# Optimization experiments

Hardware: AMD Instinct MI355X
Metric: run time of the kernel (lower is better)

The kernel has to match this reference:

```python
import jax, jax.numpy as jnp
import numpy as np

HEADS = 8
BUCKETS = 64
TEMP = 0.75
SINKHORN_ITER = 5
EPS = 1e-6


def setup_inputs() -> dict:
    key = jax.random.key(0)
    ks = jax.random.split(key, 6)
    b, t, d = 2, 4096, 1024
    x = jax.random.normal(ks[0], (b, t, d), dtype=jnp.float32)
    gumbel_u = jax.random.uniform(ks[1], (b * HEADS, BUCKETS, BUCKETS), dtype=jnp.float32)
    w_qkv = jax.random.normal(ks[2], (d, 3 * d), dtype=jnp.float32) * (d ** -0.5)
    sort_w = jax.random.normal(ks[3], (1, HEADS, (d // HEADS) * 2, BUCKETS), dtype=jnp.float32)
    w_out = jax.random.normal(ks[4], (d, d), dtype=jnp.float32) * (d ** -0.5)
    b_out = jax.random.normal(ks[5], (d,), dtype=jnp.float32) * 0.01
    return {"x": x, "gumbel_u": gumbel_u, "w_qkv": w_qkv, "sort_w": sort_w,
            "w_out": w_out, "b_out": b_out}


def reference(x, gumbel_u, w_qkv, sort_w, w_out, b_out):
    b, t, d = x.shape
    h, buckets = HEADS, BUCKETS
    d_h = d // h
    bsz = t // buckets
    bh = b * h

    # qkv projection (no bias) and head merge -> (b*h, t, d_h)
    qkv = x @ w_qkv
    q, k, v = jnp.split(qkv, 3, axis=2)
    def merge_heads(u):
        return u.reshape(b, t, h, d_h).transpose(0, 2, 1, 3).reshape(bh, t, d_h)
    q, k, v = merge_heads(q), merge_heads(k), merge_heads(v)

    # bucket -> (bh, buckets, bsz, d_h)
    b_q = q.reshape(bh, buckets, bsz, d_h)
    b_k = k.reshape(bh, buckets, bsz, d_h)
    b_v = v.reshape(bh, buckets, bsz, d_h)

    # SortNet: bucket sums -> leaky_relu(x @ W), W per-head (2*d_h, buckets)
    sx = jnp.concatenate([b_q.sum(axis=2), b_k.sum(axis=2)], axis=-1)  # (bh, buckets, 2*d_h)
    W = jnp.broadcast_to(sort_w, (b, h, 2 * d_h, buckets)).reshape(bh, 2 * d_h, buckets)
    R = jax.nn.leaky_relu(jnp.einsum('bue,bec->buc', sx, W), negative_slope=0.01)

    # gumbel-sinkhorn (log clamped for finiteness; matches torch when R >= 0)
    g = -jnp.log(-jnp.log(gumbel_u + EPS) + EPS)
    r = (jnp.log(jnp.maximum(R + EPS, EPS)) + g) / TEMP
    for _ in range(SINKHORN_ITER):
        r = r - jax.nn.logsumexp(r, axis=2, keepdims=True)
        r = r - jax.nn.logsumexp(r, axis=1, keepdims=True)
    R = jnp.exp(r)

    # zero all but top-1 along last dim
    idx = jnp.argmax(R, axis=2)
    R = jnp.where(jnp.arange(buckets)[None, None, :] == idx[..., None], R, 0.0)

    # soft-permute buckets of k and v, concat with locals -> (bh, buckets, 2*bsz, d_h)
    k_r = jnp.einsum('buv,bvtd->butd', R, b_k)
    v_r = jnp.einsum('buv,bvtd->butd', R, b_v)
    b_k2 = jnp.concatenate([k_r, b_k], axis=2)
    b_v2 = jnp.concatenate([v_r, b_v], axis=2)

    # bucketed attention; NOTE: scale uses full model dim d (as in source)
    dots = jnp.einsum('buie,buje->buij', b_q, b_k2) * (d ** -0.5)
    attn = jax.nn.softmax(dots, axis=-1)
    out = jnp.einsum('buij,buje->buie', attn, b_v2)  # (bh, buckets, bsz, d_h)

    out = out.reshape(b, h, t, d_h).transpose(0, 2, 1, 3).reshape(b, t, d)
    return out @ w_out + b_out
```

## Files before the change

kernel.cpp:

```cpp
#include <hip/hip_runtime.h>
#include <stdint.h>

#define TEMP_ 0.75f
#define EPS_ 1e-6f

typedef __attribute__((ext_vector_type(8))) short bf16x8;
typedef __attribute__((ext_vector_type(4))) float f32x4;

typedef __attribute__((address_space(1))) void gvoid_t;
typedef __attribute__((address_space(3))) void lvoid_t;

__device__ __forceinline__ void async_ld16(const void* g, void* l) {
  __builtin_amdgcn_global_load_lds((gvoid_t*)g, (lvoid_t*)l, 16, 0, 0);
}

__device__ __forceinline__ float b2f(ushort u) {
  return __builtin_bit_cast(float, (uint32_t)u << 16);
}
__device__ __forceinline__ ushort f2b(float f) {
  uint32_t x = __builtin_bit_cast(uint32_t, f);
  x += 0x7fffu + ((x >> 16) & 1u);
  return (ushort)(x >> 16);
}

__global__ __launch_bounds__(256) void prep_x(
    const float* __restrict__ x, ushort* __restrict__ xb, float* __restrict__ xsum2) {
  const int blk = blockIdx.x;
  const int bu = blk >> 1, half = blk & 1;
  const int b = bu >> 6, u = bu & 63;
  const int c = threadIdx.x * 4;
  const float* src = x + ((size_t)(b * 4096 + u * 64 + half * 32)) * 1024 + c;
  ushort* dst = xb + ((size_t)(b * 4096 + u * 64 + half * 32)) * 1024 + c;
  float s0 = 0.f, s1 = 0.f, s2 = 0.f, s3 = 0.f;
  for (int pos = 0; pos < 32; pos++) {
    float4 v = *(const float4*)(src + (size_t)pos * 1024);
    s0 += v.x; s1 += v.y; s2 += v.z; s3 += v.w;
    ushort4 o;
    o.x = f2b(v.x); o.y = f2b(v.y); o.z = f2b(v.z); o.w = f2b(v.w);
    *(ushort4*)(dst + (size_t)pos * 1024) = o;
  }
  float4 sv = {s0, s1, s2, s3};
  *(float4*)&xsum2[(size_t)blk * 1024 + c] = sv;
}

__global__ __launch_bounds__(256) void transpose_f2b(
    const float* __restrict__ src, ushort* __restrict__ dst, int R, int C) {
  __shared__ float tile[32][33];
  int bx = blockIdx.x * 32;
  int by = blockIdx.y * 32;
  int tx = threadIdx.x & 31, ty = threadIdx.x >> 5;
  #pragma unroll
  for (int i = 0; i < 32; i += 8)
    tile[ty + i][tx] = src[(size_t)(by + ty + i) * C + bx + tx];
  __syncthreads();
  #pragma unroll
  for (int i = 0; i < 32; i += 8)
    dst[(size_t)(bx + ty + i) * R + by + tx] = f2b(tile[tx][ty + i]);
}

__global__ __launch_bounds__(256) void sx_gemm_partial(
    const float* __restrict__ xsum2, const float* __restrict__ wqkv,
    float* __restrict__ SXP) {
  __shared__ float xs[128 * 8];
  const int cb = blockIdx.x;
  const int rt = blockIdx.y;
  const int kc = blockIdx.z;
  const int tid = threadIdx.x;
  for (int idx = tid; idx < 1024; idx += 256) {
    int k = idx >> 3, r = idx & 7;
    int bu = rt * 8 + r;
    int kk = kc * 128 + k;
    xs[idx] = xsum2[(size_t)(bu * 2) * 1024 + kk] + xsum2[(size_t)(bu * 2 + 1) * 1024 + kk];
  }
  __syncthreads();
  const int n = cb * 256 + tid;
  float acc[8];
  #pragma unroll
  for (int r = 0; r < 8; r++) acc[r] = 0.f;
  for (int k = 0; k < 128; k++) {
    float w = wqkv[(size_t)(kc * 128 + k) * 3072 + n];
    float4 a0 = *(const float4*)&xs[k * 8];
    float4 a1 = *(const float4*)&xs[k * 8 + 4];
    acc[0] += a0.x * w; acc[1] += a0.y * w; acc[2] += a0.z * w; acc[3] += a0.w * w;
    acc[4] += a1.x * w; acc[5] += a1.y * w; acc[6] += a1.z * w; acc[7] += a1.w * w;
  }
  #pragma unroll
  for (int r = 0; r < 8; r++)
    SXP[(size_t)(kc * 128 + rt * 8 + r) * 2048 + n] = acc[r];
}

__global__ __launch_bounds__(256) void sx_reduce(
    const float* __restrict__ SXP, float* __restrict__ SX) {
  const int bu = blockIdx.y;
  const int n = blockIdx.x * 256 + threadIdx.x;
  float s = 0.f;
  #pragma unroll
  for (int kc = 0; kc < 8; kc++)
    s += SXP[(size_t)(kc * 128 + bu) * 2048 + n];
  const int head = (n >> 7) & 7;
  const int e2 = ((n >> 10) << 7) | (n & 127);
  const int b = bu >> 6, u = bu & 63;
  SX[((size_t)((b * 8 + head) * 256) + e2) * 64 + u] = s;
}

__global__ __launch_bounds__(256) void sortnet_sinkhorn(
    const float* __restrict__ SX, const float* __restrict__ sortw,
    const float* __restrict__ gum, int* __restrict__ idxArr,
    float* __restrict__ wgtArr) {
  __shared__ float sxl[64 * 64];
  __shared__ float wl[64 * 64];
  __shared__ float rr[64 * 65];
  __shared__ float redA[256];
  __shared__ float redB[256];
  __shared__ int redi[256];
  const int bh = blockIdx.x, tid = threadIdx.x, head = bh & 7;
  const int ui = tid & 15, ci = tid >> 4;

  float acc[4][4];
  #pragma unroll
  for (int i = 0; i < 4; i++)
    #pragma unroll
    for (int j = 0; j < 4; j++) acc[i][j] = 0.f;

  const f32x4* SX4 = (const f32x4*)(SX + (size_t)bh * 16384);
  const f32x4* W4 = (const f32x4*)(sortw + (size_t)head * 16384);
  f32x4* sxl4 = (f32x4*)sxl;
  f32x4* wl4 = (f32x4*)wl;

  #pragma unroll 1
  for (int ch = 0; ch < 4; ch++) {
    __syncthreads();
    #pragma unroll 1
    for (int g = tid; g < 1024; g += 256) {
      sxl4[g] = SX4[ch * 1024 + g];
      wl4[g] = W4[ch * 1024 + g];
    }
    __syncthreads();
    #pragma unroll 2
    for (int e = 0; e < 64; e++) {
      f32x4 a = sxl4[e * 16 + ui];
      f32x4 w = wl4[e * 16 + ci];
      #pragma unroll
      for (int i = 0; i < 4; i++)
        #pragma unroll
        for (int j = 0; j < 4; j++) acc[i][j] += a[i] * w[j];
    }
  }

  #pragma unroll
  for (int i = 0; i < 4; i++)
    #pragma unroll
    for (int j = 0; j < 4; j++) {
      int u = ui * 4 + i, c = ci * 4 + j;
      float dot = acc[i][j];
      float r0 = dot > 0.f ? dot : 0.01f * dot;
      float gu = gum[(size_t)bh * 4096 + u * 64 + c];
      float inner = -logf(gu + EPS_) + EPS_;
      float g = -logf(fmaxf(inner, 1e-38f));
      rr[u * 65 + c] = (logf(fmaxf(r0 + EPS_, EPS_)) + g) / TEMP_;
    }
  __syncthreads();

  const int su = tid & 63, sq = tid >> 6;
  #pragma unroll 1
  for (int it = 0; it < 5; it++) {
    {
      float pm = -1e30f;
      #pragma unroll
      for (int j = 0; j < 16; j++) pm = fmaxf(pm, rr[su * 65 + sq * 16 + j]);
      redA[sq * 64 + su] = pm;
      __syncthreads();
      float m = fmaxf(fmaxf(redA[su], redA[64 + su]), fmaxf(redA[128 + su], redA[192 + su]));
      float ps = 0.f;
      #pragma unroll
      for (int j = 0; j < 16; j++) ps += expf(rr[su * 65 + sq * 16 + j] - m);
      redB[sq * 64 + su] = ps;
      __syncthreads();
      float l = m + logf(redB[su] + redB[64 + su] + redB[128 + su] + redB[192 + su]);
      #pragma unroll
      for (int j = 0; j < 16; j++) rr[su * 65 + sq * 16 + j] -= l;
      __syncthreads();
    }
    {
      float pm = -1e30f;
      #pragma unroll
      for (int j = 0; j < 16; j++) pm = fmaxf(pm, rr[(sq * 16 + j) * 65 + su]);
      redA[sq * 64 + su] = pm;
      __syncthreads();
      float m = fmaxf(fmaxf(redA[su], redA[64 + su]), fmaxf(redA[128 + su], redA[192 + su]));
      float ps = 0.f;
      #pragma unroll
      for (int j = 0; j < 16; j++) ps += expf(rr[(sq * 16 + j) * 65 + su] - m);
      redB[sq * 64 + su] = ps;
      __syncthreads();
      float l = m + logf(redB[su] + redB[64 + su] + redB[128 + su] + redB[192 + su]);
      #pragma unroll
      for (int j = 0; j < 16; j++) rr[(sq * 16 + j) * 65 + su] -= l;
      __syncthreads();
    }
  }

  {
    float pv = -1e30f;
    int pi = 0;
    #pragma unroll
    for (int j = 0; j < 16; j++) {
      float v = rr[su * 65 + sq * 16 + j];
      if (v > pv) { pv = v; pi = sq * 16 + j; }
    }
    redA[sq * 64 + su] = pv;
    redi[sq * 64 + su] = pi;
    __syncthreads();
    if (tid < 64) {
      float best = -1e30f;
      int bi = 0;
      #pragma unroll
      for (int q = 0; q < 4; q++) {
        float v = redA[q * 64 + tid];
        if (v > best) { best = v; bi = redi[q * 64 + tid]; }
      }
      idxArr[bh * 64 + tid] = bi;
      wgtArr[bh * 64 + tid] = expf(fminf(best, 80.f));
    }
  }
}

__global__ __launch_bounds__(256, 2) void gemm_bt(
    const ushort* __restrict__ A, const ushort* __restrict__ BT,
    int M, int N, int K, int mode,
    const float* __restrict__ bias, float* __restrict__ Cout,
    ushort* __restrict__ Qb, ushort* __restrict__ Kb, ushort* __restrict__ VT) {
  __shared__ ushort As_lo[128 * 32];
  __shared__ ushort As_hi[128 * 32];
  __shared__ ushort Bs_lo[128 * 32];
  __shared__ ushort Bs_hi[128 * 32];
  const int tid = threadIdx.x;
  const int wave = tid >> 6, lane = tid & 63;
  const int quad = lane >> 4, l16 = lane & 15;
  const int m0 = blockIdx.y * 128, n0 = blockIdx.x * 128;
  const int wm = (wave >> 1) * 64, wn = (wave & 1) * 64;

  f32x4 acc[4][4];
  #pragma unroll
  for (int i = 0; i < 4; i++)
    #pragma unroll
    for (int j = 0; j < 4; j++) acc[i][j] = (f32x4){0.f, 0.f, 0.f, 0.f};

  const int srow = wave * 32 + (lane >> 2);
  const int schunk = (lane & 3) * 8;

  for (int k0 = 0; k0 < K; k0 += 64) {
    __syncthreads();
    {
      const ushort* gA0 = A + (uint64_t)(m0 + srow) * K + k0 + schunk;
      const ushort* gB0 = BT + (uint64_t)(n0 + srow) * K + k0 + schunk;
      const int lofs = (wave * 32) * 32;
      async_ld16(gA0, (ushort*)As_lo + lofs);
      async_ld16(gA0 + (uint64_t)16 * K, (ushort*)As_lo + lofs + 16 * 32);
      async_ld16(gA0 + 32, (ushort*)As_hi + lofs);
      async_ld16(gA0 + (uint64_t)16 * K + 32, (ushort*)As_hi + lofs + 16 * 32);
      async_ld16(gB0, (ushort*)Bs_lo + lofs);
      async_ld16(gB0 + (uint64_t)16 * K, (ushort*)Bs_lo + lofs + 16 * 32);
      async_ld16(gB0 + 32, (ushort*)Bs_hi + lofs);
      async_ld16(gB0 + (uint64_t)16 * K + 32, (ushort*)Bs_hi + lofs + 16 * 32);
    }
    __syncthreads();
    #pragma unroll
    for (int kk = 0; kk < 2; kk++) {
      const ushort* Ab = kk ? As_hi : As_lo;
      const ushort* Bb = kk ? Bs_hi : Bs_lo;
      bf16x8 af[4], bfr[4];
      #pragma unroll
      for (int mt = 0; mt < 4; mt++)
        af[mt] = *(const bf16x8*)&Ab[(wm + mt * 16 + l16) * 32 + quad * 8];
      #pragma unroll
      for (int nt = 0; nt < 4; nt++)
        bfr[nt] = *(const bf16x8*)&Bb[(wn + nt * 16 + l16) * 32 + quad * 8];
      #pragma unroll
      for (int mt = 0; mt < 4; mt++)
        #pragma unroll
        for (int nt = 0; nt < 4; nt++)
          acc[mt][nt] = __builtin_amdgcn_mfma_f32_16x16x32_bf16(af[mt], bfr[nt], acc[mt][nt], 0, 0, 0);
    }
  }

  if (mode == 0) {
    #pragma unroll
    for (int mt = 0; mt < 4; mt++) {
      int row = m0 + wm + mt * 16 + quad * 4;
      #pragma unroll
      for (int nt = 0; nt < 4; nt++) {
        int col = n0 + wn + nt * 16 + l16;
        float bv = bias[col];
        #pragma unroll
        for (int r = 0; r < 4; r++)
          Cout[(uint64_t)(row + r) * N + col] = acc[mt][nt][r] + bv;
      }
    }
  } else {
    int which = blockIdx.x >> 3;
    int head = blockIdx.x & 7;
    #pragma unroll
    for (int mt = 0; mt < 4; mt++) {
      int mrow = m0 + wm + mt * 16 + quad * 4;
      int bidx = mrow >> 12;
      int ttok = mrow & 4095;
      int u = ttok >> 6, pos = ttok & 63;
      int bh = bidx * 8 + head;
      #pragma unroll
      for (int nt = 0; nt < 4; nt++) {
        int e = wn + nt * 16 + l16;
        if (which == 2) {
          ushort4 pk;
          pk.x = f2b(acc[mt][nt][0]);
          pk.y = f2b(acc[mt][nt][1]);
          pk.z = f2b(acc[mt][nt][2]);
          pk.w = f2b(acc[mt][nt][3]);
          *(ushort4*)&VT[((uint64_t)(bh * 64 + u) * 128 + e) * 64 + pos] = pk;
        } else {
          ushort* dst = (which == 0) ? Qb : Kb;
          #pragma unroll
          for (int r = 0; r < 4; r++)
            dst[((uint64_t)(bh * 64 + u) * 64 + pos + r) * 128 + e] = f2b(acc[mt][nt][r]);
        }
      }
    }
  }
}

#define KSTR 136
__global__ __launch_bounds__(256) void attn_kernel(
    const ushort* __restrict__ Qb, const ushort* __restrict__ Kb,
    const ushort* __restrict__ VT, const int* __restrict__ idxArr,
    const float* __restrict__ wgtArr, ushort* __restrict__ attn_out) {
  __shared__ ushort Qs[64 * KSTR];
  __shared__ ushort Ks[128 * KSTR];
  const int blk = blockIdx.x;
  const int u = blk & 63, bh = blk >> 6;
  const int tid = threadIdx.x, wave = tid >> 6, lane = tid & 63;
  const int quad = lane >> 4, l16 = lane & 15;
  const int vu = idxArr[bh * 64 + u] & 63;
  const float w = wgtArr[bh * 64 + u];

  const ushort* Qsrc = Qb + (uint64_t)(bh * 64 + u) * 8192;
  const ushort* Ksrc0 = Kb + (uint64_t)(bh * 64 + vu) * 8192;
  const ushort* Ksrc1 = Kb + (uint64_t)(bh * 64 + u) * 8192;
  const ushort* Vsrc0 = VT + (uint64_t)(bh * 64 + vu) * 8192;
  const ushort* Vsrc1 = VT + (uint64_t)(bh * 64 + u) * 8192;

  for (int g = tid; g < 64 * 16; g += 256) {
    int eb = g & 15, p = g >> 4;
    *(bf16x8*)&Qs[p * KSTR + eb * 8] = *(const bf16x8*)&Qsrc[p * 128 + eb * 8];
  }
  for (int g = tid; g < 128 * 16; g += 256) {
    int eb = g & 15, j = g >> 4;
    const ushort* s = (j < 64) ? &Ksrc0[j * 128 + eb * 8] : &Ksrc1[(j - 64) * 128 + eb * 8];
    *(bf16x8*)&Ks[j * KSTR + eb * 8] = *(const bf16x8*)s;
  }
  __syncthreads();

  f32x4 S[8];
  #pragma unroll
  for (int nt = 0; nt < 8; nt++) S[nt] = (f32x4){0.f, 0.f, 0.f, 0.f};
  #pragma unroll
  for (int kk = 0; kk < 4; kk++) {
    bf16x8 aq = *(const bf16x8*)&Qs[(wave * 16 + l16) * KSTR + kk * 32 + quad * 8];
    #pragma unroll
    for (int nt = 0; nt < 8; nt++) {
      bf16x8 bk = *(const bf16x8*)&Ks[(nt * 16 + l16) * KSTR + kk * 32 + quad * 8];
      S[nt] = __builtin_amdgcn_mfma_f32_16x16x32_bf16(aq, bk, S[nt], 0, 0, 0);
    }
  }
  __syncthreads();

  for (int g = tid; g < 128 * 16; g += 256) {
    int jb = g & 15, e = g >> 4;
    const ushort* s = (jb < 8) ? &Vsrc0[e * 64 + jb * 8] : &Vsrc1[e * 64 + (jb - 8) * 8];
    *(bf16x8*)&Ks[e * KSTR + jb * 8] = *(const bf16x8*)s;
  }

  const float scale = 0.03125f;
  float rowmax[4] = {-1e30f, -1e30f, -1e30f, -1e30f};
  #pragma unroll
  for (int nt = 0; nt < 8; nt++) {
    float cs = scale * ((nt < 4) ? w : 1.0f);
    #pragma unroll
    for (int r = 0; r < 4; r++) {
      S[nt][r] *= cs;
      rowmax[r] = fmaxf(rowmax[r], S[nt][r]);
    }
  }
  #pragma unroll
  for (int off = 1; off < 16; off <<= 1)
    #pragma unroll
    for (int r = 0; r < 4; r++)
      rowmax[r] = fmaxf(rowmax[r], __shfl_xor(rowmax[r], off, 64));
  float rowsum[4] = {0.f, 0.f, 0.f, 0.f};
  #pragma unroll
  for (int nt = 0; nt < 8; nt++)
    #pragma unroll
    for (int r = 0; r < 4; r++) {
      float p = expf(S[nt][r] - rowmax[r]);
      S[nt][r] = p;
      rowsum[r] += p;
    }
  #pragma unroll
  for (int off = 1; off < 16; off <<= 1)
    #pragma unroll
    for (int r = 0; r < 4; r++)
      rowsum[r] += __shfl_xor(rowsum[r], off, 64);
  float rinv[4];
  #pragma unroll
  for (int r = 0; r < 4; r++) rinv[r] = 1.0f / rowsum[r];

  #pragma unroll
  for (int nt = 0; nt < 8; nt++)
    #pragma unroll
    for (int r = 0; r < 4; r++) {
      float pv = S[nt][r] * rinv[r] * ((nt < 4) ? w : 1.0f);
      Qs[(wave * 16 + quad * 4 + r) * KSTR + nt * 16 + l16] = f2b(pv);
    }
  __syncthreads();

  f32x4 O[8];
  #pragma unroll
  for (int nt = 0; nt < 8; nt++) O[nt] = (f32x4){0.f, 0.f, 0.f, 0.f};
  #pragma unroll
  for (int kk = 0; kk < 4; kk++) {
    bf16x8 ap = *(const bf16x8*)&Qs[(wave * 16 + l16) * KSTR + kk * 32 + quad * 8];
    #pragma unroll
    for (int nt = 0; nt < 8; nt++) {
      bf16x8 bv = *(const bf16x8*)&Ks[(nt * 16 + l16) * KSTR + kk * 32 + quad * 8];
      O[nt] = __builtin_amdgcn_mfma_f32_16x16x32_bf16(ap, bv, O[nt], 0, 0, 0);
    }
  }

  const int bidx = bh >> 3, head = bh & 7;
  uint64_t rowbase =
      (uint64_t)(bidx * 4096 + u * 64 + wave * 16 + quad * 4) * 1024 + head * 128;
  #pragma unroll
  for (int nt = 0; nt < 8; nt++)
    #pragma unroll
    for (int r = 0; r < 4; r++)
      attn_out[rowbase + (uint64_t)r * 1024 + nt * 16 + l16] = f2b(O[nt][r]);
}

extern "C" void kernel_launch(void* const* d_in, const int* in_sizes, int n_in,
                              void* d_out, int out_size, void* d_ws, size_t ws_size,
                              hipStream_t stream) {
  (void)in_sizes; (void)n_in; (void)out_size; (void)ws_size;
  const float* x = (const float*)d_in[0];
  const float* gum = (const float*)d_in[1];
  const float* wqkv = (const float*)d_in[2];
  const float* sortw = (const float*)d_in[3];
  const float* wout = (const float*)d_in[4];
  const float* bout = (const float*)d_in[5];
  float* out = (float*)d_out;

  char* ws = (char*)d_ws;
  size_t off = 0;
  auto alloc = [&](size_t bytes) {
    char* p = ws + off;
    off += (bytes + 255) & ~(size_t)255;
    return p;
  };
  ushort* xb = (ushort*)alloc((size_t)8192 * 1024 * 2);
  float* xsum2 = (float*)alloc((size_t)256 * 1024 * 4);
  ushort* wqkvT = (ushort*)alloc((size_t)3072 * 1024 * 2);
  ushort* woutT = (ushort*)alloc((size_t)1024 * 1024 * 2);
  float* SX = (float*)alloc((size_t)16 * 256 * 64 * 4);
  ushort* Qb = (ushort*)alloc((size_t)16 * 64 * 64 * 128 * 2);
  ushort* Kb = (ushort*)alloc((size_t)16 * 64 * 64 * 128 * 2);
  ushort* VT = (ushort*)alloc((size_t)16 * 64 * 128 * 64 * 2);
  int* idxArr = (int*)alloc((size_t)16 * 64 * 4);
  float* wgtArr = (float*)alloc((size_t)16 * 64 * 4);
  ushort* attn = xb;
  float* SXP = (float*)Qb;

  prep_x<<<256, 256, 0, stream>>>(x, xb, xsum2);
  transpose_f2b<<<dim3(3072 / 32, 1024 / 32), 256, 0, stream>>>(wqkv, wqkvT, 1024, 3072);
  transpose_f2b<<<dim3(1024 / 32, 1024 / 32), 256, 0, stream>>>(wout, woutT, 1024, 1024);
  sx_gemm_partial<<<dim3(8, 16, 8), 256, 0, stream>>>(xsum2, wqkv, SXP);
  sx_reduce<<<dim3(8, 128), 256, 0, stream>>>(SXP, SX);
  sortnet_sinkhorn<<<16, 256, 0, stream>>>(SX, sortw, gum, idxArr, wgtArr);
  gemm_bt<<<dim3(3072 / 128, 8192 / 128), 256, 0, stream>>>(
      xb, wqkvT, 8192, 3072, 1024, 1, nullptr, nullptr, Qb, Kb, VT);
  attn_kernel<<<16 * 64, 256, 0, stream>>>(Qb, Kb, VT, idxArr, wgtArr, attn);
  gemm_bt<<<dim3(1024 / 128, 8192 / 128), 256, 0, stream>>>(
      attn, woutT, 8192, 1024, 1024, 0, bout, out, nullptr, nullptr, nullptr);
}
```

Measured before the change: 264.7 us.

## Add 256x256-tile double-buffered QKV GEMM with swizzled LDS and MFMA interleave

Replaces the generic 128x128 gemm_bt launch for the QKV projection with a dedicated 512-thread kernel that computes 256x256 output tiles. It double-buffers A and B in LDS using async global-to-LDS loads with an XOR swizzle, and splits each K step into four MFMA phases. The phases are separated by barriers and priority bumps so the next tile's loads overlap compute. The larger tile raises operand reuse per byte loaded. In exchange it uses 128KB of LDS per block, limiting occupancy to one block per CU, and its 384 blocks form a partial second wave.

Result: slower. 281.6 us (+6.4%).

```diff
diff --git a/kernel.cpp b/kernel.cpp
--- a/kernel.cpp
+++ b/kernel.cpp
@@ -323,6 +323,165 @@
           for (int r = 0; r < 4; r++)
             dst[((uint64_t)(bh * 64 + u) * 64 + pos + r) * 128 + e] = f2b(acc[mt][nt][r]);
         }
+      }
+    }
+  }
+}
+
+#define GK 1024
+
+__device__ __forceinline__ void stage256(const ushort* __restrict__ G, int k0,
+                                         ushort* lds, int wv, int ln) {
+  #pragma unroll
+  for (int q = 0; q < 4; ++q) {
+    int p = q * 512 + wv * 64 + ln;
+    int row = p >> 3;
+    int cc = (p & 7) ^ (((row >> 2) & 1) << 1);
+    async_ld16(G + (size_t)row * GK + k0 + cc * 8,
+               lds + (size_t)(q * 512 + wv * 64) * 8);
+  }
+}
+
+__device__ __forceinline__ bf16x8 ldfrag(const ushort* buf, int row, int kc) {
+  int pc = kc ^ (((row >> 2) & 1) << 1);
+  return *(const bf16x8*)&buf[row * 64 + pc * 8];
+}
+
+__global__ __launch_bounds__(512, 2) void gemm256_qkv(
+    const ushort* __restrict__ A, const ushort* __restrict__ BT,
+    ushort* __restrict__ Qb, ushort* __restrict__ Kb, ushort* __restrict__ VT) {
+  __shared__ ushort As0[256 * 64];
+  __shared__ ushort As1[256 * 64];
+  __shared__ ushort Bs0[256 * 64];
+  __shared__ ushort Bs1[256 * 64];
+  const int tid = threadIdx.x;
+  const int wv = tid >> 6, ln = tid & 63;
+  const int quad = ln >> 4, l16 = ln & 15;
+  const int wm = (wv >> 2) * 128;
+  const int wn = (wv & 3) * 64;
+  const int m0 = blockIdx.y * 256, n0 = blockIdx.x * 256;
+  const ushort* Ag = A + (size_t)m0 * GK;
+  const ushort* Bg = BT + (size_t)n0 * GK;
+
+  f32x4 acc[8][4];
+  #pragma unroll
+  for (int i = 0; i < 8; i++)
+    #pragma unroll
+    for (int j = 0; j < 4; j++) acc[i][j] = (f32x4){0.f, 0.f, 0.f, 0.f};
+
+  stage256(Ag, 0, As0, wv, ln);
+  stage256(Bg, 0, Bs0, wv, ln);
+  __syncthreads();
+
+  #pragma unroll 1
+  for (int t = 0; t < GK / 64; ++t) {
+    ushort* Ab = (t & 1) ? As1 : As0;
+    ushort* Bb = (t & 1) ? Bs1 : Bs0;
+    ushort* An = (t & 1) ? As0 : As1;
+    ushort* Bn = (t & 1) ? Bs0 : Bs1;
+    const int kn = (t + 1) * 64;
+    bf16x8 a0[4][2], a1[4][2], b0[2][2], b1[2][2];
+
+    #pragma unroll
+    for (int mt = 0; mt < 4; ++mt)
+      #pragma unroll
+      for (int kk = 0; kk < 2; ++kk)
+        a0[mt][kk] = ldfrag(Ab, wm + mt * 16 + l16, kk * 4 + quad);
+    #pragma unroll
+    for (int nt = 0; nt < 2; ++nt)
+      #pragma unroll
+      for (int kk = 0; kk < 2; ++kk)
+        b0[nt][kk] = ldfrag(Bb, wn + nt * 16 + l16, kk * 4 + quad);
+    if (t < GK / 64 - 1) stage256(Ag, kn, An, wv, ln);
+    __builtin_amdgcn_s_barrier();
+    __builtin_amdgcn_s_setprio(1);
+    #pragma unroll
+    for (int mt = 0; mt < 4; ++mt)
+      #pragma unroll
+      for (int nt = 0; nt < 2; ++nt)
+        #pragma unroll
+        for (int kk = 0; kk < 2; ++kk)
+          acc[mt][nt] = __builtin_amdgcn_mfma_f32_16x16x32_bf16(a0[mt][kk], b0[nt][kk], acc[mt][nt], 0, 0, 0);
+    __builtin_amdgcn_s_setprio(0);
+    __builtin_amdgcn_s_barrier();
+
+    #pragma unroll
+    for (int nt = 0; nt < 2; ++nt)
+      #pragma unroll
+      for (int kk = 0; kk < 2; ++kk)
+        b1[nt][kk] = ldfrag(Bb, wn + (2 + nt) * 16 + l16, kk * 4 + quad);
+    if (t < GK / 64 - 1) stage256(Bg, kn, Bn, wv, ln);
+    __builtin_amdgcn_s_barrier();
+    __builtin_amdgcn_s_setprio(1);
+    #pragma unroll
+    for (int mt = 0; mt < 4; ++mt)
+      #pragma unroll
+      for (int nt = 0; nt < 2; ++nt)
+        #pragma unroll
+        for (int kk = 0; kk < 2; ++kk)
+          acc[mt][2 + nt] = __builtin_amdgcn_mfma_f32_16x16x32_bf16(a0[mt][kk], b1[nt][kk], acc[mt][2 + nt], 0, 0, 0);
+    __builtin_amdgcn_s_setprio(0);
+    __builtin_amdgcn_s_barrier();
+
+    #pragma unroll
+    for (int mt = 0; mt < 4; ++mt)
+      #pragma unroll
+      for (int kk = 0; kk < 2; ++kk)
+        a1[mt][kk] = ldfrag(Ab, wm + 64 + mt * 16 + l16, kk * 4 + quad);
+    __builtin_amdgcn_s_barrier();
+    __builtin_amdgcn_s_setprio(1);
+    #pragma unroll
+    for (int mt = 0; mt < 4; ++mt)
+      #pragma unroll
+      for (int nt = 0; nt < 2; ++nt)
+        #pragma unroll
+        for (int kk = 0; kk < 2; ++kk)
+          acc[4 + mt][2 + nt] = __builtin_amdgcn_mfma_f32_16x16x32_bf16(a1[mt][kk], b1[nt][kk], acc[4 + mt][2 + nt], 0, 0, 0);
+    __builtin_amdgcn_s_setprio(0);
+    __builtin_amdgcn_s_barrier();
+
+    #pragma unroll
+    for (int nt = 0; nt < 2; ++nt)
+      #pragma unroll
+      for (int kk = 0; kk < 2; ++kk)
+        b0[nt][kk] = ldfrag(Bb, wn + nt * 16 + l16, kk * 4 + quad);
+    __builtin_amdgcn_s_setprio(1);
+    #pragma unroll
+    for (int mt = 0; mt < 4; ++mt)
+      #pragma unroll
+      for (int nt = 0; nt < 2; ++nt)
+        #pragma unroll
+        for (int kk = 0; kk < 2; ++kk)
+          acc[4 + mt][nt] = __builtin_amdgcn_mfma_f32_16x16x32_bf16(a1[mt][kk], b0[nt][kk], acc[4 + mt][nt], 0, 0, 0);
+    __builtin_amdgcn_s_setprio(0);
+    __syncthreads();
+  }
+
+  const int which = n0 >> 10;
+  #pragma unroll
+  for (int mt = 0; mt < 8; ++mt) {
+    int mrow = m0 + wm + mt * 16 + quad * 4;
+    int bidx = mrow >> 12;
+    int ttok = mrow & 4095;
+    int u = ttok >> 6, pos = ttok & 63;
+    #pragma unroll
+    for (int nt = 0; nt < 4; ++nt) {
+      int col = n0 + wn + nt * 16 + l16;
+      int head = (col >> 7) & 7;
+      int e = col & 127;
+      int bh = bidx * 8 + head;
+      if (which == 2) {
+        ushort4 pk;
+        pk.x = f2b(acc[mt][nt][0]);
+        pk.y = f2b(acc[mt][nt][1]);
+        pk.z = f2b(acc[mt][nt][2]);
+        pk.w = f2b(acc[mt][nt][3]);
+        *(ushort4*)&VT[((uint64_t)(bh * 64 + u) * 128 + e) * 64 + pos] = pk;
+      } else {
+        ushort* dst = (which == 0) ? Qb : Kb;
+        #pragma unroll
+        for (int r = 0; r < 4; ++r)
+          dst[((uint64_t)(bh * 64 + u) * 64 + pos + r) * 128 + e] = f2b(acc[mt][nt][r]);
       }
     }
   }
@@ -483,8 +642,7 @@
   sx_gemm_partial<<<dim3(8, 16, 8), 256, 0, stream>>>(xsum2, wqkv, SXP);
   sx_reduce<<<dim3(8, 128), 256, 0, stream>>>(SXP, SX);
   sortnet_sinkhorn<<<16, 256, 0, stream>>>(SX, sortw, gum, idxArr, wgtArr);
-  gemm_bt<<<dim3(3072 / 128, 8192 / 128), 256, 0, stream>>>(
-      xb, wqkvT, 8192, 3072, 1024, 1, nullptr, nullptr, Qb, Kb, VT);
+  gemm256_qkv<<<dim3(3072 / 256, 8192 / 256), 512, 0, stream>>>(xb, wqkvT, Qb, Kb, VT);
   attn_kernel<<<16 * 64, 256, 0, stream>>>(Qb, Kb, VT, idxArr, wgtArr, attn);
   gemm_bt<<<dim3(1024 / 128, 8192 / 128), 256, 0, stream>>>(
       attn, woutT, 8192, 1024, 1024, 0, bout, out, nullptr, nullptr, nullptr);
```

## Add 256x256-tile QKV GEMM with 4-stage async LDS pipeline

Applied to the files above, without the earlier changes.

Replaces the generic 128x128 gemm_bt launch for the QKV projection with a dedicated kernel. It uses 256x256 output tiles, 512 threads and a 4-deep ring of direct global-to-LDS loads, with XOR-swizzled LDS rows and raised wave priority around the MFMA block. The bigger tiles increase operand reuse per byte loaded, and the deeper prefetch hides memory latency. In exchange it needs about 128KB of LDS per block, which limits a CU to one block. The grid also shrinks to 384 blocks, which may leave a partial tail wave across the CUs.

After: 290.1 us. +9.6%, slower.

```diff
diff --git a/kernel.cpp b/kernel.cpp
--- a/kernel.cpp
+++ b/kernel.cpp
@@ -323,6 +323,119 @@
           for (int r = 0; r < 4; r++)
             dst[((uint64_t)(bh * 64 + u) * 64 + pos + r) * 128 + e] = f2b(acc[mt][nt][r]);
         }
+      }
+    }
+  }
+}
+
+#define GK 1024
+
+__device__ __forceinline__ void stage32(const ushort* __restrict__ G, int k0,
+                                        ushort* lds, int wv, int ln) {
+  #pragma unroll
+  for (int q = 0; q < 2; ++q) {
+    int p = q * 512 + wv * 64 + ln;
+    int row = p >> 2;
+    int cc = (p & 3) ^ ((row >> 1) & 3);
+    async_ld16(G + (size_t)row * GK + k0 + cc * 8,
+               lds + (size_t)(q * 512 + wv * 64) * 8);
+  }
+}
+
+__device__ __forceinline__ bf16x8 ldfrag32(const ushort* buf, int row, int q) {
+  int pc = q ^ ((row >> 1) & 3);
+  return *(const bf16x8*)&buf[row * 32 + pc * 8];
+}
+
+__global__ __launch_bounds__(512, 2) void gemm256_qkv(
+    const ushort* __restrict__ A, const ushort* __restrict__ BT,
+    ushort* __restrict__ Qb, ushort* __restrict__ Kb, ushort* __restrict__ VT) {
+  __shared__ ushort As[4][256 * 32];
+  __shared__ ushort Bs[4][256 * 32];
+  const int tid = threadIdx.x;
+  const int wv = tid >> 6, ln = tid & 63;
+  const int quad = ln >> 4, l16 = ln & 15;
+  const int wm = (wv >> 2) * 128;
+  const int wn = (wv & 3) * 64;
+  const int m0 = blockIdx.y * 256, n0 = blockIdx.x * 256;
+  const ushort* Ag = A + (size_t)m0 * GK;
+  const ushort* Bg = BT + (size_t)n0 * GK;
+
+  f32x4 acc[8][4];
+  #pragma unroll
+  for (int i = 0; i < 8; i++)
+    #pragma unroll
+    for (int j = 0; j < 4; j++) acc[i][j] = (f32x4){0.f, 0.f, 0.f, 0.f};
+
+  auto tile = [&](int t) {
+    const ushort* Ab = As[t & 3];
+    const ushort* Bb = Bs[t & 3];
+    bf16x8 a[8], b[4];
+    #pragma unroll
+    for (int mt = 0; mt < 8; ++mt)
+      a[mt] = ldfrag32(Ab, wm + mt * 16 + l16, quad);
+    #pragma unroll
+    for (int nt = 0; nt < 4; ++nt)
+      b[nt] = ldfrag32(Bb, wn + nt * 16 + l16, quad);
+    __builtin_amdgcn_s_setprio(1);
+    #pragma unroll
+    for (int mt = 0; mt < 8; ++mt)
+      #pragma unroll
+      for (int nt = 0; nt < 4; ++nt)
+        acc[mt][nt] = __builtin_amdgcn_mfma_f32_16x16x32_bf16(a[mt], b[nt], acc[mt][nt], 0, 0, 0);
+    __builtin_amdgcn_s_setprio(0);
+  };
+
+  stage32(Ag, 0, As[0], wv, ln);
+  stage32(Bg, 0, Bs[0], wv, ln);
+  stage32(Ag, 32, As[1], wv, ln);
+  stage32(Bg, 32, Bs[1], wv, ln);
+  stage32(Ag, 64, As[2], wv, ln);
+  stage32(Bg, 64, Bs[2], wv, ln);
+
+  #pragma unroll 1
+  for (int t = 0; t < 30; ++t) {
+    asm volatile("s_waitcnt vmcnt(8)\n\ts_barrier" ::: "memory");
+    __builtin_amdgcn_sched_barrier(0);
+    if (t < 29) {
+      int tn = t + 3;
+      stage32(Ag, tn * 32, As[tn & 3], wv, ln);
+      stage32(Bg, tn * 32, Bs[tn & 3], wv, ln);
+    }
+    tile(t);
+  }
+  asm volatile("s_waitcnt vmcnt(4)\n\ts_barrier" ::: "memory");
+  __builtin_amdgcn_sched_barrier(0);
+  tile(30);
+  asm volatile("s_waitcnt vmcnt(0)\n\ts_barrier" ::: "memory");
+  __builtin_amdgcn_sched_barrier(0);
+  tile(31);
+
+  const int which = n0 >> 10;
+  #pragma unroll
+  for (int mt = 0; mt < 8; ++mt) {
+    int mrow = m0 + wm + mt * 16 + quad * 4;
+    int bidx = mrow >> 12;
+    int ttok = mrow & 4095;
+    int u = ttok >> 6, pos = ttok & 63;
+    #pragma unroll
+    for (int nt = 0; nt < 4; ++nt) {
+      int col = n0 + wn + nt * 16 + l16;
+      int head = (col >> 7) & 7;
+      int e = col & 127;
+      int bh = bidx * 8 + head;
+      if (which == 2) {
+        ushort4 pk;
+        pk.x = f2b(acc[mt][nt][0]);
+        pk.y = f2b(acc[mt][nt][1]);
+        pk.z = f2b(acc[mt][nt][2]);
+        pk.w = f2b(acc[mt][nt][3]);
+        *(ushort4*)&VT[((uint64_t)(bh * 64 + u) * 128 + e) * 64 + pos] = pk;
+      } else {
+        ushort* dst = (which == 0) ? Qb : Kb;
+        #pragma unroll
+        for (int r = 0; r < 4; ++r)
+          dst[((uint64_t)(bh * 64 + u) * 64 + pos + r) * 128 + e] = f2b(acc[mt][nt][r]);
       }
     }
   }
@@ -483,8 +596,7 @@
   sx_gemm_partial<<<dim3(8, 16, 8), 256, 0, stream>>>(xsum2, wqkv, SXP);
   sx_reduce<<<dim3(8, 128), 256, 0, stream>>>(SXP, SX);
   sortnet_sinkhorn<<<16, 256, 0, stream>>>(SX, sortw, gum, idxArr, wgtArr);
-  gemm_bt<<<dim3(3072 / 128, 8192 / 128), 256, 0, stream>>>(
-      xb, wqkvT, 8192, 3072, 1024, 1, nullptr, nullptr, Qb, Kb, VT);
+  gemm256_qkv<<<dim3(3072 / 256, 8192 / 256), 512, 0, stream>>>(xb, wqkvT, Qb, Kb, VT);
   attn_kernel<<<16 * 64, 256, 0, stream>>>(Qb, Kb, VT, idxArr, wgtArr, attn);
   gemm_bt<<<dim3(1024 / 128, 8192 / 128), 256, 0, stream>>>(
       attn, woutT, 8192, 1024, 1024, 0, bout, out, nullptr, nullptr, nullptr);
```

## Double-buffer GEMM LDS tiles with XOR swizzle and async prefetch two tiles ahead

Applied to the files above, without the earlier changes.

The bf16 GEMM main loop moves from a single-buffered LDS tile with two barriers per k-step to a two-stage double buffer. Global-to-LDS async loads for tile t+2 are issued while tile t is computed, with vmcnt-based waits. The LDS layout becomes a 128x64 tile with an XOR swizzle to avoid bank conflicts on ds_read_b128. It also adds inline asm LDS reads and s_setprio around the MFMA block. LDS use doubles to 64KB per block, which may reduce occupancy below the declared 2 blocks per CU, and the hand-written waitcnt logic is fragile.

Result: slower. 271.2 us (+2.5%).

```diff
diff --git a/kernel.cpp b/kernel.cpp
--- a/kernel.cpp
+++ b/kernel.cpp
@@ -21,6 +21,16 @@
   uint32_t x = __builtin_bit_cast(uint32_t, f);
   x += 0x7fffu + ((x >> 16) & 1u);
   return (ushort)(x >> 16);
+}
+
+__device__ __forceinline__ uint32_t lds_u32(const void* p) {
+  return (uint32_t)(uintptr_t)(lvoid_t*)p;
+}
+
+__device__ __forceinline__ bf16x8 dsr(uint32_t addr) {
+  bf16x8 d;
+  asm volatile("ds_read_b128 %0, %1" : "=v"(d) : "v"(addr));
+  return d;
 }
 
 __global__ __launch_bounds__(256) void prep_x(
@@ -230,15 +240,39 @@
     int M, int N, int K, int mode,
     const float* __restrict__ bias, float* __restrict__ Cout,
     ushort* __restrict__ Qb, ushort* __restrict__ Kb, ushort* __restrict__ VT) {
-  __shared__ ushort As_lo[128 * 32];
-  __shared__ ushort As_hi[128 * 32];
-  __shared__ ushort Bs_lo[128 * 32];
-  __shared__ ushort Bs_hi[128 * 32];
+  __shared__ ushort As[2][128 * 64];
+  __shared__ ushort Bs[2][128 * 64];
   const int tid = threadIdx.x;
   const int wave = tid >> 6, lane = tid & 63;
   const int quad = lane >> 4, l16 = lane & 15;
   const int m0 = blockIdx.y * 128, n0 = blockIdx.x * 128;
   const int wm = (wave >> 1) * 64, wn = (wave & 1) * 64;
+  const ushort* Ap = A + (uint64_t)m0 * K;
+  const ushort* Bp = BT + (uint64_t)n0 * K;
+
+  auto stage = [&](const ushort* G, int k0, ushort* buf) {
+    #pragma unroll
+    for (int q = 0; q < 4; ++q) {
+      int p = q * 256 + tid;
+      int row = p >> 3, pp = p & 7;
+      int cc = pp ^ (row & 7);
+      async_ld16(G + (uint64_t)row * K + k0 + cc * 8,
+                 buf + (q * 256 + wave * 64) * 8);
+    }
+  };
+
+  const uint32_t asB = lds_u32(&As[0][0]);
+  const uint32_t bsB = lds_u32(&Bs[0][0]);
+  uint32_t aoff[2][4], boff[2][4];
+  #pragma unroll
+  for (int kk = 0; kk < 2; ++kk) {
+    int pc = (kk * 4 + quad) ^ (l16 & 7);
+    #pragma unroll
+    for (int mt = 0; mt < 4; ++mt) {
+      aoff[kk][mt] = (uint32_t)((wm + mt * 16 + l16) * 128 + pc * 16);
+      boff[kk][mt] = (uint32_t)((wn + mt * 16 + l16) * 128 + pc * 16);
+    }
+  }
 
   f32x4 acc[4][4];
   #pragma unroll
@@ -246,41 +280,44 @@
     #pragma unroll
     for (int j = 0; j < 4; j++) acc[i][j] = (f32x4){0.f, 0.f, 0.f, 0.f};
 
-  const int srow = wave * 32 + (lane >> 2);
-  const int schunk = (lane & 3) * 8;
-
-  for (int k0 = 0; k0 < K; k0 += 64) {
-    __syncthreads();
-    {
-      const ushort* gA0 = A + (uint64_t)(m0 + srow) * K + k0 + schunk;
-      const ushort* gB0 = BT + (uint64_t)(n0 + srow) * K + k0 + schunk;
-      const int lofs = (wave * 32) * 32;
-      async_ld16(gA0, (ushort*)As_lo + lofs);
-      async_ld16(gA0 + (uint64_t)16 * K, (ushort*)As_lo + lofs + 16 * 32);
-      async_ld16(gA0 + 32, (ushort*)As_hi + lofs);
-      async_ld16(gA0 + (uint64_t)16 * K + 32, (ushort*)As_hi + lofs + 16 * 32);
-      async_ld16(gB0, (ushort*)Bs_lo + lofs);
-      async_ld16(gB0 + (uint64_t)16 * K, (ushort*)Bs_lo + lofs + 16 * 32);
-      async_ld16(gB0 + 32, (ushort*)Bs_hi + lofs);
-      async_ld16(gB0 + (uint64_t)16 * K + 32, (ushort*)Bs_hi + lofs + 16 * 32);
-    }
-    __syncthreads();
-    #pragma unroll
-    for (int kk = 0; kk < 2; kk++) {
-      const ushort* Ab = kk ? As_hi : As_lo;
-      const ushort* Bb = kk ? Bs_hi : Bs_lo;
-      bf16x8 af[4], bfr[4];
-      #pragma unroll
-      for (int mt = 0; mt < 4; mt++)
-        af[mt] = *(const bf16x8*)&Ab[(wm + mt * 16 + l16) * 32 + quad * 8];
-      #pragma unroll
-      for (int nt = 0; nt < 4; nt++)
-        bfr[nt] = *(const bf16x8*)&Bb[(wn + nt * 16 + l16) * 32 + quad * 8];
-      #pragma unroll
-      for (int mt = 0; mt < 4; mt++)
+  const int NT = K >> 6;
+  stage(Ap, 0, As[0]);
+  stage(Bp, 0, Bs[0]);
+  stage(Ap, 64, As[1]);
+  stage(Bp, 64, Bs[1]);
+
+  #pragma unroll 1
+  for (int t = 0; t < NT; ++t) {
+    if (t < NT - 1)
+      asm volatile("s_waitcnt vmcnt(8)\n\ts_barrier" ::: "memory");
+    else
+      asm volatile("s_waitcnt vmcnt(0)\n\ts_barrier" ::: "memory");
+
+    const uint32_t ab = asB + (uint32_t)(t & 1) * 16384u;
+    const uint32_t bb = bsB + (uint32_t)(t & 1) * 16384u;
+    bf16x8 a[2][4], b[2][4];
+    #pragma unroll
+    for (int kk = 0; kk < 2; ++kk) {
+      #pragma unroll
+      for (int mt = 0; mt < 4; ++mt) a[kk][mt] = dsr(ab + aoff[kk][mt]);
+      #pragma unroll
+      for (int nt = 0; nt < 4; ++nt) b[kk][nt] = dsr(bb + boff[kk][nt]);
+    }
+    asm volatile("s_waitcnt lgkmcnt(0)" ::: "memory");
+    __builtin_amdgcn_sched_barrier(0);
+    __builtin_amdgcn_s_setprio(1);
+    #pragma unroll
+    for (int kk = 0; kk < 2; ++kk)
+      #pragma unroll
+      for (int mt = 0; mt < 4; ++mt)
         #pragma unroll
-        for (int nt = 0; nt < 4; nt++)
-          acc[mt][nt] = __builtin_amdgcn_mfma_f32_16x16x32_bf16(af[mt], bfr[nt], acc[mt][nt], 0, 0, 0);
+        for (int nt = 0; nt < 4; ++nt)
+          acc[mt][nt] = __builtin_amdgcn_mfma_f32_16x16x32_bf16(a[kk][mt], b[kk][nt], acc[mt][nt], 0, 0, 0);
+    __builtin_amdgcn_s_setprio(0);
+    asm volatile("s_barrier" ::: "memory");
+    if (t + 2 < NT) {
+      stage(Ap, (t + 2) * 64, As[t & 1]);
+      stage(Bp, (t + 2) * 64, Bs[t & 1]);
     }
   }
 
```
